# Kernel tuning notes

Hardware: AMD Instinct MI355X
Metric: run time of the kernel (lower is better)

The kernel has to match this reference:

```python
import jax, jax.numpy as jnp
import numpy as np


def _relative_index(ih: int, iw: int) -> np.ndarray:
    # Static precompute mirroring the torch buffer.
    yy, xx = np.meshgrid(np.arange(ih), np.arange(iw), indexing='ij')
    coords = np.stack([yy.ravel(), xx.ravel()])                 # [2, n]
    rel = coords[:, :, None] - coords[:, None, :]               # [2, n, n]
    rel[0] += ih - 1
    rel[1] += iw - 1
    rel[0] *= 2 * iw - 1
    return rel.sum(0).ravel()                                   # [n*n]


def setup_inputs() -> dict:
    key = jax.random.key(0)
    ks = jax.random.split(key, 5)
    B, N, INP, OUP, HEADS = 64, 256, 512, 512, 16
    ih = iw = 16
    return {
        'x': jax.random.normal(ks[0], (B, N, INP), jnp.float32),
        'w_qkv': jax.random.normal(ks[1], (INP, 3 * OUP), jnp.float32) * 0.02,
        'rel_bias_table': jax.random.normal(ks[2], ((2 * ih - 1) * (2 * iw - 1), HEADS), jnp.float32) * 0.02,
        'w_out': jax.random.normal(ks[3], (OUP, OUP), jnp.float32) * 0.02,
        'b_out': jax.random.normal(ks[4], (OUP,), jnp.float32) * 0.02,
        'ih': ih,
        'iw': iw,
    }


def reference(x, w_qkv, rel_bias_table, w_out, b_out, ih, iw):
    B, N, _ = x.shape
    heads = rel_bias_table.shape[1]
    oup = w_out.shape[0]
    dim_head = oup // heads
    scale = dim_head ** -0.5

    qkv = jnp.einsum('bni,ij->bnj', x, w_qkv)                   # [B, N, 3*oup]
    q, k, v = jnp.split(qkv, 3, axis=-1)
    split_heads = lambda t: t.reshape(B, N, heads, dim_head).transpose(0, 2, 1, 3)
    q, k, v = split_heads(q), split_heads(k), split_heads(v)    # [B, H, N, D]

    dots = jnp.einsum('bhnd,bhmd->bhnm', q, k) * scale          # [B, H, N, N]
    rel_idx = jnp.asarray(_relative_index(int(ih), int(iw)))    # [N*N]
    bias = rel_bias_table[rel_idx].reshape(N, N, heads)         # gather
    dots = dots + bias.transpose(2, 0, 1)[None]                 # [1, H, N, N]

    attn = jax.nn.softmax(dots, axis=-1)
    out = jnp.einsum('bhnm,bhmd->bhnd', attn, v)                # [B, H, N, D]
    out = out.transpose(0, 2, 1, 3).reshape(B, N, oup)
    return jnp.einsum('bno,op->bnp', out, w_out.T) + b_out
```

## Files before the change

kernel.cpp:

```cpp
#include <hip/hip_runtime.h>
#include <stdint.h>

typedef unsigned short u16;
typedef unsigned int u32;
typedef __attribute__((ext_vector_type(8))) __bf16 bf16x8;
typedef __attribute__((ext_vector_type(2))) u32 u32x2;
typedef __attribute__((ext_vector_type(4))) u32 u32x4;
typedef __attribute__((ext_vector_type(4))) float f32x4;

__device__ __forceinline__ float bf2f(u16 x) { return __uint_as_float(((u32)x) << 16); }
__device__ __forceinline__ u16 f2bf(float f) {
  u32 u = __float_as_uint(f);
  u32 r = (u + 0x7fffu + ((u >> 16) & 1u)) >> 16;
  return (u16)r;
}

__device__ __forceinline__ u32x2 ld8(const u16* p) { return *(const u32x2*)p; }
__device__ __forceinline__ u32x4 ld16(const u16* p) { return *(const u32x4*)p; }
__device__ __forceinline__ bf16x8 mk_frag(u32x2 lo, u32x2 hi) {
  union { bf16x8 v; u32x2 u[2]; } t;
  t.u[0] = lo; t.u[1] = hi;
  return t.v;
}

__device__ __forceinline__ void stage_fm(u16* lds, int ch, u32x4 v) {
  int row = ch >> 2, q = ch & 3;
  int base = (row >> 4) * 512 + (row & 15) * 8;
  int col0 = q * 8;
  int col1 = q * 8 + 4;
  int d0 = base + (((col0 & 15) >> 2) * 128) + ((col0 >> 4) * 4);
  int d1 = base + (((col1 & 15) >> 2) * 128) + ((col1 >> 4) * 4);
  u32x2 h0; h0.x = v.x; h0.y = v.y;
  u32x2 h1; h1.x = v.z; h1.y = v.w;
  *(u32x2*)&lds[d0] = h0;
  *(u32x2*)&lds[d1] = h1;
}

__device__ __forceinline__ bf16x8 frag_fm(const u16* lds, int subtile, int g, int c) {
  union { bf16x8 v; u32x4 u; } t;
  t.u = ld16(&lds[subtile * 512 + g * 128 + c * 8]);
  return t.v;
}

__global__ void probe_dtype(const u32* __restrict__ x, u32* __restrict__ flag) {
  if (threadIdx.x == 0 && blockIdx.x == 0) {
    int cnt = 0;
    for (int i = 0; i < 32; ++i) {
      u32 e = (x[i] >> 7) & 0xffu;
      cnt += (e >= 96u && e <= 140u) ? 1 : 0;
    }
    *flag = (cnt == 32) ? 1u : 0u;
  }
}

__global__ __launch_bounds__(256) void conv4(const void* __restrict__ src, u16* __restrict__ dst,
                                             const u32* __restrict__ flag, int n4) {
  const bool isbf = (*flag != 0u);
  const int stride = gridDim.x * 256;
  for (int i = blockIdx.x * 256 + threadIdx.x; i < n4; i += stride) {
    if (isbf) {
      ((u32x2*)dst)[i] = ((const u32x2*)src)[i];
    } else {
      const float* s = (const float*)src + (size_t)i * 4;
      u32x2 o;
      o.x = (u32)f2bf(s[0]) | ((u32)f2bf(s[1]) << 16);
      o.y = (u32)f2bf(s[2]) | ((u32)f2bf(s[3]) << 16);
      ((u32x2*)dst)[i] = o;
    }
  }
}

__global__ __launch_bounds__(256) void bias_prep(const void* __restrict__ table,
                                                 float* __restrict__ biasT,
                                                 const u32* __restrict__ flag) {
  const bool isbf = (*flag != 0u);
  int i = blockIdx.x * 256 + threadIdx.x;
  if (i < 16 * 961) {
    int h = i / 961, idx = i - h * 961;
    biasT[i] = isbf ? bf2f(((const u16*)table)[idx * 16 + h])
                    : ((const float*)table)[idx * 16 + h];
  }
}

__global__ __launch_bounds__(256) void transpose_dt(const void* __restrict__ in,
                                                    u16* __restrict__ out,
                                                    const u32* __restrict__ flag, int R, int C) {
  __shared__ u16 t[32][33];
  const bool isbf = (*flag != 0u);
  int r0 = blockIdx.y * 32, c0 = blockIdx.x * 32;
  int rr = threadIdx.x >> 5, cc = threadIdx.x & 31;
#pragma unroll
  for (int i = 0; i < 4; ++i) {
    size_t idx = (size_t)(r0 + rr + i * 8) * C + c0 + cc;
    t[rr + i * 8][cc] = isbf ? ((const u16*)in)[idx] : f2bf(((const float*)in)[idx]);
  }
  __syncthreads();
#pragma unroll
  for (int i = 0; i < 4; ++i) out[(size_t)(c0 + rr + i * 8) * R + r0 + cc] = t[cc][rr + i * 8];
}

__global__ __launch_bounds__(256) void gemm128(const u16* __restrict__ A,
                                               const u16* __restrict__ BT,
                                               u16* __restrict__ O, int K, int ldo) {
  __shared__ u16 As[128 * 32];
  __shared__ u16 Bs[128 * 32];
  const int tid = threadIdx.x;
  const int wave = tid >> 6, lane = tid & 63;
  const int c = lane & 15, g = lane >> 4;
  const int wm = wave >> 1, wn = wave & 1;
  const int bn = blockIdx.x, bm = blockIdx.y;

  const u16* Ab = A + (size_t)bm * 128 * K;
  const u16* Bb = BT + (size_t)bn * 128 * K;

  f32x4 acc[4][4] = {};
  const int row0 = tid >> 2, q0 = tid & 3;
  const int row1 = (tid + 256) >> 2;

  for (int k0 = 0; k0 < K; k0 += 32) {
    u32x4 a0 = ld16(Ab + (size_t)row0 * K + k0 + q0 * 8);
    u32x4 b0 = ld16(Bb + (size_t)row0 * K + k0 + q0 * 8);
    u32x4 a1 = ld16(Ab + (size_t)row1 * K + k0 + q0 * 8);
    u32x4 b1 = ld16(Bb + (size_t)row1 * K + k0 + q0 * 8);
    __syncthreads();
    stage_fm(As, tid, a0);
    stage_fm(Bs, tid, b0);
    stage_fm(As, tid + 256, a1);
    stage_fm(Bs, tid + 256, b1);
    __syncthreads();
    bf16x8 af[4], bfr[4];
#pragma unroll
    for (int i = 0; i < 4; ++i) {
      af[i] = frag_fm(As, wm * 4 + i, g, c);
      bfr[i] = frag_fm(Bs, wn * 4 + i, g, c);
    }
#pragma unroll
    for (int i = 0; i < 4; ++i)
#pragma unroll
      for (int j = 0; j < 4; ++j)
        acc[i][j] = __builtin_amdgcn_mfma_f32_16x16x32_bf16(af[i], bfr[j], acc[i][j], 0, 0, 0);
  }

#pragma unroll
  for (int i = 0; i < 4; ++i)
#pragma unroll
    for (int j = 0; j < 4; ++j) {
      int jg = bn * 128 + wn * 64 + j * 16 + c;
#pragma unroll
      for (int r = 0; r < 4; ++r) {
        int mg = bm * 128 + wm * 64 + i * 16 + 4 * g + r;
        O[(size_t)mg * ldo + jg] = f2bf(acc[i][j][r]);
      }
    }
}

__global__ __launch_bounds__(256) void gemm_final(const u16* __restrict__ A,
                                                  const u16* __restrict__ BT,
                                                  const u16* __restrict__ bias,
                                                  void* __restrict__ O, int row0g,
                                                  const u32* __restrict__ flag) {
  __shared__ u16 As[128 * 32];
  __shared__ u16 Bs[128 * 32];
  const int K = 512;
  const bool isbf = (*flag != 0u);
  const int tid = threadIdx.x;
  const int wave = tid >> 6, lane = tid & 63;
  const int c = lane & 15, g = lane >> 4;
  const int wm = wave >> 1, wn = wave & 1;
  const int bn = blockIdx.x, bm = blockIdx.y;

  const u16* Ab = A + (size_t)bm * 128 * K;
  const u16* Bb = BT + (size_t)bn * 128 * K;

  f32x4 acc[4][4] = {};
  const int row0 = tid >> 2, q0 = tid & 3;
  const int row1 = (tid + 256) >> 2;

  for (int k0 = 0; k0 < K; k0 += 32) {
    u32x4 a0 = ld16(Ab + (size_t)row0 * K + k0 + q0 * 8);
    u32x4 b0 = ld16(Bb + (size_t)row0 * K + k0 + q0 * 8);
    u32x4 a1 = ld16(Ab + (size_t)row1 * K + k0 + q0 * 8);
    u32x4 b1 = ld16(Bb + (size_t)row1 * K + k0 + q0 * 8);
    __syncthreads();
    stage_fm(As, tid, a0);
    stage_fm(Bs, tid, b0);
    stage_fm(As, tid + 256, a1);
    stage_fm(Bs, tid + 256, b1);
    __syncthreads();
    bf16x8 af[4], bfr[4];
#pragma unroll
    for (int i = 0; i < 4; ++i) {
      af[i] = frag_fm(As, wm * 4 + i, g, c);
      bfr[i] = frag_fm(Bs, wn * 4 + i, g, c);
    }
#pragma unroll
    for (int i = 0; i < 4; ++i)
#pragma unroll
      for (int j = 0; j < 4; ++j)
        acc[i][j] = __builtin_amdgcn_mfma_f32_16x16x32_bf16(af[i], bfr[j], acc[i][j], 0, 0, 0);
  }

#pragma unroll
  for (int i = 0; i < 4; ++i)
#pragma unroll
    for (int j = 0; j < 4; ++j) {
      int jg = bn * 128 + wn * 64 + j * 16 + c;
      float bv = bf2f(bias[jg]);
#pragma unroll
      for (int r = 0; r < 4; ++r) {
        int mg = bm * 128 + wm * 64 + i * 16 + 4 * g + r;
        float v = acc[i][j][r] + bv;
        size_t off = (size_t)(row0g + mg) * 512 + jg;
        if (isbf) ((u16*)O)[off] = f2bf(v);
        else ((float*)O)[off] = v;
      }
    }
}

__global__ __launch_bounds__(256) void attn_kernel(const u16* __restrict__ qkv,
                                                   const float* __restrict__ biasT,
                                                   u16* __restrict__ Out) {
  __shared__ u16 smem[26624];
  float* biasS = (float*)&smem[16384];

  const int tid = threadIdx.x;
  const int wave = tid >> 6, lane = tid & 63;
  const int c = lane & 15, g = lane >> 4;
  const int h = blockIdx.x & 15, b = blockIdx.x >> 4;

  const u16* xb = qkv + (size_t)b * 256 * 1536;

  u32x4 kvr[4];
#pragma unroll
  for (int i = 0; i < 4; ++i) {
    int ch = tid + i * 256;
    int m = ch >> 2;
    kvr[i] = ld16(xb + (size_t)m * 1536 + 512 + h * 32 + (ch & 3) * 8);
  }
#pragma unroll
  for (int i = 0; i < 4; ++i) stage_fm(smem, tid + i * 256, kvr[i]);

#pragma unroll
  for (int i = 0; i < 16; ++i) {
    int e2 = tid + i * 256;
    int n = e2 >> 4, d = (e2 & 15) * 2;
    u32 val = *(const u32*)(xb + (size_t)n * 1536 + 1024 + h * 32 + d);
    smem[8192 + d * 256 + (n ^ (8 * (d & 7)))] = (u16)(val & 0xffffu);
    smem[8192 + (d + 1) * 256 + (n ^ (8 * ((d + 1) & 7)))] = (u16)(val >> 16);
  }
  for (int i = tid; i < 961; i += 256) biasS[i] = biasT[h * 961 + i];
  __syncthreads();

  const u16* Vt = &smem[8192];
  u16* Pw = &smem[18432 + wave * 2048];
  const float scale = 0.17677669529663687f;
  const int xa = (8 * (c & 7)) ^ ((c & 8) >> 1);
  const int va = 8 * (c & 7);

  for (int rg = 0; rg < 4; ++rg) {
    const int qrow = rg * 64 + wave * 16 + c;
    const u16* qp = xb + (size_t)qrow * 1536 + h * 32 + 4 * g;
    bf16x8 qf = mk_frag(ld8(qp), ld8(qp + 16));

    f32x4 s[16];
#pragma unroll
    for (int f = 0; f < 16; ++f) {
      bf16x8 kf = frag_fm(smem, f, g, c);
      f32x4 z = {0.f, 0.f, 0.f, 0.f};
      s[f] = __builtin_amdgcn_mfma_f32_16x16x32_bf16(qf, kf, z, 0, 0, 0);
    }

    const int nb = rg * 64 + wave * 16 + 4 * g;
#pragma unroll
    for (int f = 0; f < 16; ++f) {
      int mcol = f * 16 + c;
      int y2 = mcol >> 4, x2 = mcol & 15;
#pragma unroll
      for (int j = 0; j < 4; ++j) {
        int n = nb + j;
        s[f][j] = s[f][j] * scale + biasS[((n >> 4) - y2 + 15) * 31 + ((n & 15) - x2 + 15)];
      }
    }

    float inv[4];
#pragma unroll
    for (int j = 0; j < 4; ++j) {
      float m = s[0][j];
#pragma unroll
      for (int f = 1; f < 16; ++f) m = fmaxf(m, s[f][j]);
      m = fmaxf(m, __shfl_xor(m, 1, 64));
      m = fmaxf(m, __shfl_xor(m, 2, 64));
      m = fmaxf(m, __shfl_xor(m, 4, 64));
      m = fmaxf(m, __shfl_xor(m, 8, 64));
      float sm = 0.f;
#pragma unroll
      for (int f = 0; f < 16; ++f) {
        float e = __expf(s[f][j] - m);
        s[f][j] = e;
        sm += e;
      }
      sm += __shfl_xor(sm, 1, 64);
      sm += __shfl_xor(sm, 2, 64);
      sm += __shfl_xor(sm, 4, 64);
      sm += __shfl_xor(sm, 8, 64);
      inv[j] = 1.0f / sm;
    }

    f32x4 o0 = {0.f, 0.f, 0.f, 0.f}, o1 = {0.f, 0.f, 0.f, 0.f};
#pragma unroll
    for (int half = 0; half < 2; ++half) {
#pragma unroll
      for (int f = half * 8; f < half * 8 + 8; ++f) {
        int col = f * 16 + c - half * 128;
#pragma unroll
        for (int j = 0; j < 4; ++j) {
          int row = 4 * g + j;
          int sw = (8 * (row & 7)) ^ ((row & 8) >> 1);
          Pw[row * 128 + (col ^ sw)] = f2bf(s[f][j]);
        }
      }
#pragma unroll
      for (int kb = 0; kb < 4; ++kb) {
        int kc = kb * 32;
        int kg = half * 128 + kc;
        bf16x8 pf = mk_frag(ld8(&Pw[c * 128 + ((kc + 4 * g) ^ xa)]),
                            ld8(&Pw[c * 128 + ((kc + 16 + 4 * g) ^ xa)]));
        bf16x8 v0 = mk_frag(ld8(&Vt[c * 256 + ((kg + 4 * g) ^ va)]),
                            ld8(&Vt[c * 256 + ((kg + 16 + 4 * g) ^ va)]));
        bf16x8 v1 = mk_frag(ld8(&Vt[(16 + c) * 256 + ((kg + 4 * g) ^ va)]),
                            ld8(&Vt[(16 + c) * 256 + ((kg + 16 + 4 * g) ^ va)]));
        o0 = __builtin_amdgcn_mfma_f32_16x16x32_bf16(pf, v0, o0, 0, 0, 0);
        o1 = __builtin_amdgcn_mfma_f32_16x16x32_bf16(pf, v1, o1, 0, 0, 0);
      }
    }

#pragma unroll
    for (int j = 0; j < 4; ++j) {
      int n = nb + j;
      size_t off = ((size_t)b * 256 + n) * 512 + h * 32;
      Out[off + c] = f2bf(o0[j] * inv[j]);
      Out[off + 16 + c] = f2bf(o1[j] * inv[j]);
    }
  }
}

extern "C" void kernel_launch(void* const* d_in, const int* in_sizes, int n_in, void* d_out,
                              int out_size, void* d_ws, size_t ws_size, hipStream_t stream) {
  (void)in_sizes; (void)n_in; (void)out_size;
  const void* x = d_in[0];
  const void* w_qkv = d_in[1];
  const void* table = d_in[2];
  const void* w_out = d_in[3];
  const void* b_out = d_in[4];

  char* ws = (char*)d_ws;
  u32* flag = (u32*)ws;
  u16* xc = (u16*)(ws + 256);
  u16* wqkvT = (u16*)(ws + 16777472);
  float* biasT = (float*)(ws + 18350336);
  u16* woC = (u16*)(ws + 18411840);
  u16* bC = (u16*)(ws + 18936128);
  const size_t DYN = 18937344;
  int CB = 64;
  while (CB > 1 && DYN + (size_t)CB * 1048576 > ws_size) CB >>= 1;
  u16* qkv = (u16*)(ws + DYN);
  u16* att = (u16*)(ws + DYN + (size_t)CB * 786432);

  dim3 blk(256);
  probe_dtype<<<dim3(1), dim3(64), 0, stream>>>((const u32*)x, flag);
  conv4<<<dim3(2048), blk, 0, stream>>>(x, xc, flag, 2097152);
  conv4<<<dim3(256), blk, 0, stream>>>(w_out, woC, flag, 65536);
  conv4<<<dim3(1), blk, 0, stream>>>(b_out, bC, flag, 128);
  bias_prep<<<dim3(61), blk, 0, stream>>>(table, biasT, flag);
  transpose_dt<<<dim3(48, 16), blk, 0, stream>>>(w_qkv, wqkvT, flag, 512, 1536);

  for (int s0 = 0; s0 < 64; s0 += CB) {
    const u16* xcc = xc + (size_t)s0 * 256 * 512;
    gemm128<<<dim3(12, CB * 2), blk, 0, stream>>>(xcc, wqkvT, qkv, 512, 1536);
    attn_kernel<<<dim3(CB * 16), blk, 0, stream>>>(qkv, biasT, att);
    gemm_final<<<dim3(4, CB * 2), blk, 0, stream>>>(att, woC, bC, d_out, s0 * 256, flag);
  }
}
```

Before: 143.4 us.

## Keep attention probabilities in registers via transposed QK MFMA, exp2 softmax

Swaps the MFMA operands for QK^T so each lane's score accumulator already matches the A-operand layout of the PV MFMA. This lets the probabilities be packed straight into bf16 fragments with no LDS round trip, removing the per-wave P buffer and shrinking shared memory. Softmax now works per lane column with a tree reduction and cross-group shuffles. It uses exp2 with log2e folded into the bias table and scale, and normalises P before the PV product. Normalising before the PV product rounds P to bf16 after scaling, which changes the precision slightly.

```diff
diff --git a/kernel.cpp b/kernel.cpp
--- a/kernel.cpp
+++ b/kernel.cpp
@@ -13,6 +13,9 @@
   u32 u = __float_as_uint(f);
   u32 r = (u + 0x7fffu + ((u >> 16) & 1u)) >> 16;
   return (u16)r;
+}
+__device__ __forceinline__ u32 pk2(float a, float b) {
+  return (u32)f2bf(a) | ((u32)f2bf(b) << 16);
 }
 
 __device__ __forceinline__ u32x2 ld8(const u16* p) { return *(const u32x2*)p; }
@@ -77,8 +80,9 @@
   int i = blockIdx.x * 256 + threadIdx.x;
   if (i < 16 * 961) {
     int h = i / 961, idx = i - h * 961;
-    biasT[i] = isbf ? bf2f(((const u16*)table)[idx * 16 + h])
-                    : ((const float*)table)[idx * 16 + h];
+    float v = isbf ? bf2f(((const u16*)table)[idx * 16 + h])
+                   : ((const float*)table)[idx * 16 + h];
+    biasT[i] = v * 1.4426950408889634f;
   }
 }
 
@@ -220,7 +224,7 @@
 __global__ __launch_bounds__(256) void attn_kernel(const u16* __restrict__ qkv,
                                                    const float* __restrict__ biasT,
                                                    u16* __restrict__ Out) {
-  __shared__ u16 smem[26624];
+  __shared__ u16 smem[18432];
   float* biasS = (float*)&smem[16384];
 
   const int tid = threadIdx.x;
@@ -252,10 +256,8 @@
   __syncthreads();
 
   const u16* Vt = &smem[8192];
-  u16* Pw = &smem[18432 + wave * 2048];
-  const float scale = 0.17677669529663687f;
-  const int xa = (8 * (c & 7)) ^ ((c & 8) >> 1);
   const int va = 8 * (c & 7);
+  const float scale2 = 0.25503484f;
 
   for (int rg = 0; rg < 4; ++rg) {
     const int qrow = rg * 64 + wave * 16 + c;
@@ -267,79 +269,73 @@
     for (int f = 0; f < 16; ++f) {
       bf16x8 kf = frag_fm(smem, f, g, c);
       f32x4 z = {0.f, 0.f, 0.f, 0.f};
-      s[f] = __builtin_amdgcn_mfma_f32_16x16x32_bf16(qf, kf, z, 0, 0, 0);
+      s[f] = __builtin_amdgcn_mfma_f32_16x16x32_bf16(kf, qf, z, 0, 0, 0);
+    }
+
+    const int ybase = rg * 4 + wave;
+#pragma unroll
+    for (int f = 0; f < 16; ++f) {
+      const float* bp = &biasS[(ybase - f + 15) * 31 + c + 15 - 4 * g];
+#pragma unroll
+      for (int j = 0; j < 4; ++j) s[f][j] = s[f][j] * scale2 + bp[-j];
+    }
+
+    float t[16];
+#pragma unroll
+    for (int f = 0; f < 16; ++f)
+      t[f] = fmaxf(fmaxf(s[f][0], s[f][1]), fmaxf(s[f][2], s[f][3]));
+#pragma unroll
+    for (int st = 8; st > 0; st >>= 1)
+#pragma unroll
+      for (int f = 0; f < 8; ++f)
+        if (f < st) t[f] = fmaxf(t[f], t[f + st]);
+    float mx = t[0];
+    mx = fmaxf(mx, __shfl_xor(mx, 16, 64));
+    mx = fmaxf(mx, __shfl_xor(mx, 32, 64));
+
+    float u[16];
+#pragma unroll
+    for (int f = 0; f < 16; ++f) {
+#pragma unroll
+      for (int j = 0; j < 4; ++j) s[f][j] = __builtin_amdgcn_exp2f(s[f][j] - mx);
+      u[f] = (s[f][0] + s[f][1]) + (s[f][2] + s[f][3]);
+    }
+#pragma unroll
+    for (int st = 8; st > 0; st >>= 1)
+#pragma unroll
+      for (int f = 0; f < 8; ++f)
+        if (f < st) u[f] += u[f + st];
+    float sm = u[0];
+    sm += __shfl_xor(sm, 16, 64);
+    sm += __shfl_xor(sm, 32, 64);
+    const float invc = __builtin_amdgcn_rcpf(sm);
+
+    f32x4 o0 = {0.f, 0.f, 0.f, 0.f}, o1 = {0.f, 0.f, 0.f, 0.f};
+#pragma unroll
+    for (int kb = 0; kb < 8; ++kb) {
+      const int f0 = 2 * kb, f1 = 2 * kb + 1;
+      u32x2 lo, hi;
+      lo.x = pk2(s[f0][0] * invc, s[f0][1] * invc);
+      lo.y = pk2(s[f0][2] * invc, s[f0][3] * invc);
+      hi.x = pk2(s[f1][0] * invc, s[f1][1] * invc);
+      hi.y = pk2(s[f1][2] * invc, s[f1][3] * invc);
+      bf16x8 pf = mk_frag(lo, hi);
+      const int kg = kb * 32;
+      bf16x8 v0 = mk_frag(ld8(&Vt[c * 256 + ((kg + 4 * g) ^ va)]),
+                          ld8(&Vt[c * 256 + ((kg + 16 + 4 * g) ^ va)]));
+      bf16x8 v1 = mk_frag(ld8(&Vt[(16 + c) * 256 + ((kg + 4 * g) ^ va)]),
+                          ld8(&Vt[(16 + c) * 256 + ((kg + 16 + 4 * g) ^ va)]));
+      o0 = __builtin_amdgcn_mfma_f32_16x16x32_bf16(pf, v0, o0, 0, 0, 0);
+      o1 = __builtin_amdgcn_mfma_f32_16x16x32_bf16(pf, v1, o1, 0, 0, 0);
     }
 
     const int nb = rg * 64 + wave * 16 + 4 * g;
-#pragma unroll
-    for (int f = 0; f < 16; ++f) {
-      int mcol = f * 16 + c;
-      int y2 = mcol >> 4, x2 = mcol & 15;
-#pragma unroll
-      for (int j = 0; j < 4; ++j) {
-        int n = nb + j;
-        s[f][j] = s[f][j] * scale + biasS[((n >> 4) - y2 + 15) * 31 + ((n & 15) - x2 + 15)];
-      }
-    }
-
-    float inv[4];
-#pragma unroll
-    for (int j = 0; j < 4; ++j) {
-      float m = s[0][j];
-#pragma unroll
-      for (int f = 1; f < 16; ++f) m = fmaxf(m, s[f][j]);
-      m = fmaxf(m, __shfl_xor(m, 1, 64));
-      m = fmaxf(m, __shfl_xor(m, 2, 64));
-      m = fmaxf(m, __shfl_xor(m, 4, 64));
-      m = fmaxf(m, __shfl_xor(m, 8, 64));
-      float sm = 0.f;
-#pragma unroll
-      for (int f = 0; f < 16; ++f) {
-        float e = __expf(s[f][j] - m);
-        s[f][j] = e;
-        sm += e;
-      }
-      sm += __shfl_xor(sm, 1, 64);
-      sm += __shfl_xor(sm, 2, 64);
-      sm += __shfl_xor(sm, 4, 64);
-      sm += __shfl_xor(sm, 8, 64);
-      inv[j] = 1.0f / sm;
-    }
-
-    f32x4 o0 = {0.f, 0.f, 0.f, 0.f}, o1 = {0.f, 0.f, 0.f, 0.f};
-#pragma unroll
-    for (int half = 0; half < 2; ++half) {
-#pragma unroll
-      for (int f = half * 8; f < half * 8 + 8; ++f) {
-        int col = f * 16 + c - half * 128;
-#pragma unroll
-        for (int j = 0; j < 4; ++j) {
-          int row = 4 * g + j;
-          int sw = (8 * (row & 7)) ^ ((row & 8) >> 1);
-          Pw[row * 128 + (col ^ sw)] = f2bf(s[f][j]);
-        }
-      }
-#pragma unroll
-      for (int kb = 0; kb < 4; ++kb) {
-        int kc = kb * 32;
-        int kg = half * 128 + kc;
-        bf16x8 pf = mk_frag(ld8(&Pw[c * 128 + ((kc + 4 * g) ^ xa)]),
-                            ld8(&Pw[c * 128 + ((kc + 16 + 4 * g) ^ xa)]));
-        bf16x8 v0 = mk_frag(ld8(&Vt[c * 256 + ((kg + 4 * g) ^ va)]),
-                            ld8(&Vt[c * 256 + ((kg + 16 + 4 * g) ^ va)]));
-        bf16x8 v1 = mk_frag(ld8(&Vt[(16 + c) * 256 + ((kg + 4 * g) ^ va)]),
-                            ld8(&Vt[(16 + c) * 256 + ((kg + 16 + 4 * g) ^ va)]));
-        o0 = __builtin_amdgcn_mfma_f32_16x16x32_bf16(pf, v0, o0, 0, 0, 0);
-        o1 = __builtin_amdgcn_mfma_f32_16x16x32_bf16(pf, v1, o1, 0, 0, 0);
-      }
-    }
-
 #pragma unroll
     for (int j = 0; j < 4; ++j) {
       int n = nb + j;
       size_t off = ((size_t)b * 256 + n) * 512 + h * 32;
-      Out[off + c] = f2bf(o0[j] * inv[j]);
-      Out[off + 16 + c] = f2bf(o1[j] * inv[j]);
+      Out[off + c] = f2bf(o0[j]);
+      Out[off + 16 + c] = f2bf(o1[j]);
     }
   }
 }
```

Result: no change. 142.9 us (-0.4%).
